# Kernel optimization log

Hardware: AMD Instinct MI355X
Metric: run time of the kernel (lower is better)

The kernel has to match this reference:

```python
import jax, jax.numpy as jnp
import numpy as np

N_NODES = 100000
N_EDGES = 1600000
N_GRAPHS = 128
IN_FEATS = 128
OUT_FEATS = 64


def setup_inputs() -> dict:
    key = jax.random.key(0)
    k1, k2, k3, k4, k5, k6 = jax.random.split(key, 6)
    features = jax.random.normal(k1, (N_NODES, IN_FEATS), jnp.float32)
    src = jax.random.randint(k2, (N_EDGES,), 0, N_NODES, dtype=jnp.int32)
    dst = jax.random.randint(k3, (N_EDGES,), 0, N_NODES, dtype=jnp.int32)
    graph_ids = jnp.sort(jax.random.randint(k4, (N_NODES,), 0, N_GRAPHS, dtype=jnp.int32))
    # Xavier-uniform init as in DGL GraphConv
    lim1 = float(np.sqrt(6.0 / (IN_FEATS + IN_FEATS)))
    lim2 = float(np.sqrt(6.0 / (IN_FEATS + OUT_FEATS)))
    W1 = jax.random.uniform(k5, (IN_FEATS, IN_FEATS), jnp.float32, -lim1, lim1)
    W2 = jax.random.uniform(k6, (IN_FEATS, OUT_FEATS), jnp.float32, -lim2, lim2)
    b1 = jnp.zeros((IN_FEATS,), jnp.float32)
    b2 = jnp.zeros((OUT_FEATS,), jnp.float32)
    return {"features": features, "W1": W1, "b1": b1, "W2": W2, "b2": b2,
            "src": src, "dst": dst, "graph_ids": graph_ids, "num_graphs": N_GRAPHS}


def _graph_conv(x, W, b, src, dst, n_nodes):
    # DGL GraphConv, norm='both': D_dst^{-1/2} A D_src^{-1/2} X W + b
    ones = jnp.ones(src.shape, x.dtype)
    deg_out = jax.ops.segment_sum(ones, src, num_segments=n_nodes)
    deg_in = jax.ops.segment_sum(ones, dst, num_segments=n_nodes)
    norm_src = jax.lax.rsqrt(jnp.maximum(deg_out, 1.0))  # [N]
    norm_dst = jax.lax.rsqrt(jnp.maximum(deg_in, 1.0))   # [N]
    h = (x * norm_src[:, None]) @ W                       # dense transform first
    agg = jax.ops.segment_sum(h[src], dst, num_segments=n_nodes)  # spmm-style scatter-add
    return agg * norm_dst[:, None] + b


def reference(features, W1, b1, W2, b2, src, dst, graph_ids, num_graphs):
    n = features.shape[0]
    h = jax.nn.relu(_graph_conv(features, W1, b1, src, dst, n))
    h = jax.nn.relu(_graph_conv(h, W2, b2, src, dst, n))
    # dgl.mean_nodes: per-graph mean over nodes
    sums = jax.ops.segment_sum(h, graph_ids, num_segments=num_graphs)
    counts = jax.ops.segment_sum(jnp.ones((n, 1), h.dtype), graph_ids, num_segments=num_graphs)
    return sums / jnp.maximum(counts, 1.0)
```

## Files before the change

### kernel.cpp

```cpp
#include <hip/hip_runtime.h>
#include <hip/hip_bf16.h>


#define NPP_SHIFT 9
#define NPP 512
#define MAXP 256
#define NB 512

typedef __attribute__((ext_vector_type(8))) short frag8;
typedef __attribute__((ext_vector_type(4))) float f32x4;
typedef __attribute__((ext_vector_type(2))) float v2f;

__launch_bounds__(256)
__global__ void passA_count(const int* __restrict__ src, const int* __restrict__ dst,
                            int E, int P, int* __restrict__ counts_src,
                            int* __restrict__ counts_dst,
                            const int* __restrict__ gids, int N, int G,
                            int* __restrict__ gcnt) {
    __shared__ int h1[MAXP], h2[MAXP], h3[MAXP];
    int tid = threadIdx.x;
    for (int i = tid; i < MAXP; i += 256) { h1[i] = 0; h2[i] = 0; h3[i] = 0; }
    __syncthreads();
    int per_block = (E + NB - 1) / NB;
    int e0 = blockIdx.x * per_block;
    int e1 = min(e0 + per_block, E);
    for (int e = e0 + tid; e < e1; e += 256) {
        atomicAdd(&h1[src[e] >> NPP_SHIFT], 1);
        atomicAdd(&h2[dst[e] >> NPP_SHIFT], 1);
    }
    int npb = (N + NB - 1) / NB;
    int n0 = blockIdx.x * npb;
    int n1 = min(n0 + npb, N);
    for (int i = n0 + tid; i < n1; i += 256) atomicAdd(&h3[gids[i]], 1);
    __syncthreads();
    for (int i = tid; i < P; i += 256) {
        counts_src[(size_t)blockIdx.x * P + i] = h1[i];
        counts_dst[(size_t)blockIdx.x * P + i] = h2[i];
    }
    for (int i = tid; i < G; i += 256)
        if (h3[i]) atomicAdd(&gcnt[i], h3[i]);
}

__launch_bounds__(1024)
__global__ void scanB(const int* __restrict__ counts, int* __restrict__ offs,
                      int* __restrict__ ptot, int P) {
    __shared__ int s[1024];
    int tid = threadIdx.x;
    int p = blockIdx.x % P;
    int st = blockIdx.x / P;
    const int* c = counts + (size_t)st * NB * P;
    int v = (tid < NB) ? c[(size_t)tid * P + p] : 0;
    s[tid] = v;
    __syncthreads();
    for (int off = 1; off < 1024; off <<= 1) {
        int t = (tid >= off) ? s[tid - off] : 0;
        __syncthreads();
        s[tid] += t;
        __syncthreads();
    }
    if (tid < NB) offs[(size_t)st * NB * P + (size_t)tid * P + p] = s[tid] - v;
    if (tid == 1023) ptot[st * P + p] = s[1023];
}

__launch_bounds__(256)
__global__ void passC_scatter(const int* __restrict__ src, const int* __restrict__ dst,
                              int E, int P, const int* __restrict__ offs,
                              const int* __restrict__ ptot, int* __restrict__ pbase,
                              int* __restrict__ ebuf_src, int2* __restrict__ ebuf_dst) {
    __shared__ int cur1[MAXP], cur2[MAXP], sc[256];
    int tid = threadIdx.x;
    int v = (tid < P) ? ptot[tid] : 0;
    sc[tid] = v;
    __syncthreads();
    for (int off = 1; off < 256; off <<= 1) {
        int t = (tid >= off) ? sc[tid - off] : 0;
        __syncthreads();
        sc[tid] += t;
        __syncthreads();
    }
    int base0 = sc[tid] - v;
    if (tid < P) {
        cur1[tid] = base0 + offs[(size_t)blockIdx.x * P + tid];
        if (blockIdx.x == 0) pbase[tid] = base0;
    }
    __syncthreads();
    v = (tid < P) ? ptot[P + tid] : 0;
    sc[tid] = v;
    __syncthreads();
    for (int off = 1; off < 256; off <<= 1) {
        int t = (tid >= off) ? sc[tid - off] : 0;
        __syncthreads();
        sc[tid] += t;
        __syncthreads();
    }
    int base1 = sc[tid] - v;
    if (tid < P) {
        cur2[tid] = base1 + offs[(size_t)NB * P + (size_t)blockIdx.x * P + tid];
        if (blockIdx.x == 0) pbase[P + tid] = base1;
    }
    __syncthreads();
    int per_block = (E + NB - 1) / NB;
    int e0 = blockIdx.x * per_block;
    int e1 = min(e0 + per_block, E);
    for (int e = e0 + tid; e < e1; e += 256) {
        int s = src[e];
        int d = dst[e];
        int pos1 = atomicAdd(&cur1[s >> NPP_SHIFT], 1);
        ebuf_src[pos1] = s;
        int pos2 = atomicAdd(&cur2[d >> NPP_SHIFT], 1);
        ebuf_dst[pos2] = make_int2(d, s);
    }
}

__launch_bounds__(512)
__global__ void passD_build(const int* __restrict__ ebuf_src, const int2* __restrict__ ebuf_dst,
                            const int* __restrict__ ptot, const int* __restrict__ pbase,
                            float* __restrict__ norm_src, int* __restrict__ row_start,
                            int* __restrict__ csr_src, int N, int E, int P) {
    __shared__ int hs[NPP], hd[NPP], sc[NPP];
    int tid = threadIdx.x;
    int p = blockIdx.x;
    int node_lo = p << NPP_SHIFT;
    int nl = min(NPP, N - node_lo);
    hs[tid] = 0;
    hd[tid] = 0;
    __syncthreads();
    int nsrc = ptot[p];
    int base_s = pbase[p];
    for (int i = tid; i < nsrc; i += 512)
        atomicAdd(&hs[ebuf_src[base_s + i] - node_lo], 1);
    int ndst = ptot[P + p];
    int base_d = pbase[P + p];
    for (int i = tid; i < ndst; i += 512)
        atomicAdd(&hd[ebuf_dst[base_d + i].x - node_lo], 1);
    __syncthreads();
    if (tid < nl) norm_src[node_lo + tid] = rsqrtf((float)max(hs[tid], 1));
    int myh = hd[tid];
    sc[tid] = myh;
    __syncthreads();
    for (int off = 1; off < 512; off <<= 1) {
        int t = (tid >= off) ? sc[tid - off] : 0;
        __syncthreads();
        sc[tid] += t;
        __syncthreads();
    }
    int row0 = base_d + sc[tid] - myh;
    if (tid < nl) row_start[node_lo + tid] = row0;
    if (p == P - 1 && tid == 0) row_start[N] = E;
    __syncthreads();
    hd[tid] = row0;
    __syncthreads();
    for (int i = tid; i < ndst; i += 512) {
        int2 r = ebuf_dst[base_d + i];
        int pos = atomicAdd(&hd[r.x - node_lo], 1);
        csr_src[pos] = r.y;
    }
}

template <int COLS, bool BF16IN, bool PERM, bool FP8OUT>
__launch_bounds__(256)
__global__ void gemm_mfma(const void* __restrict__ xin, const float* __restrict__ w,
                          const float* __restrict__ norm,
                          void* __restrict__ out, int n) {
    constexpr int NT = COLS / 16;
    __shared__ short wlds[4 * NT * 64 * 8];
    const int tid = threadIdx.x;
    for (int i = tid; i < 128 * COLS / 4; i += 256) {
        int k = (i * 4) / COLS;
        int n0 = (i * 4) % COLS;
        float4 wv;
        if constexpr (PERM) {
            int ksrc = 64 * ((k >> 2) & 1) + 16 * (k & 3) + (k >> 3);
            wv = *reinterpret_cast<const float4*>(w + (size_t)ksrc * COLS + n0);
        } else {
            wv = reinterpret_cast<const float4*>(w)[i];
        }
        int c = k >> 5, q = (k >> 3) & 3, j = k & 7;
        float vals[4] = {wv.x, wv.y, wv.z, wv.w};
#pragma unroll
        for (int u = 0; u < 4; ++u) {
            int nn = n0 + u;
            int t = nn >> 4;
            int ln = (q << 4) | (nn & 15);
            union { __hip_bfloat16 b; short s; } cv;
            cv.b = __float2bfloat16(vals[u]);
            wlds[(((c * NT + t) << 6) | ln) * 8 + j] = cv.s;
        }
    }
    __syncthreads();

    const int lane = tid & 63;
    const int wid = tid >> 6;
    const int m = lane & 15;
    const int q = lane >> 4;
    const int ntiles = (n + 15) >> 4;
    const frag8* wfr = reinterpret_cast<const frag8*>(wlds);

    for (int wt = blockIdx.x * 4 + wid; wt < ntiles; wt += gridDim.x * 4) {
        const int row = (wt << 4) + m;
        frag8 af[4];
        if (row < n) {
            if constexpr (BF16IN) {
                const frag8* xp = reinterpret_cast<const frag8*>(
                    (const __hip_bfloat16*)xin + (size_t)row * 128);
#pragma unroll
                for (int c = 0; c < 4; ++c) af[c] = xp[c * 4 + q];
            } else {
                const float* xp = (const float*)xin + (size_t)row * 128;
                float nm = norm[row];
#pragma unroll
                for (int c = 0; c < 4; ++c) {
                    int base = c * 32 + q * 8;
                    float4 v0 = *reinterpret_cast<const float4*>(xp + base);
                    float4 v1 = *reinterpret_cast<const float4*>(xp + base + 4);
                    union { frag8 f; short s[8]; } a;
                    union { __hip_bfloat16 b; short s; } cv;
                    cv.b = __float2bfloat16(v0.x * nm); a.s[0] = cv.s;
                    cv.b = __float2bfloat16(v0.y * nm); a.s[1] = cv.s;
                    cv.b = __float2bfloat16(v0.z * nm); a.s[2] = cv.s;
                    cv.b = __float2bfloat16(v0.w * nm); a.s[3] = cv.s;
                    cv.b = __float2bfloat16(v1.x * nm); a.s[4] = cv.s;
                    cv.b = __float2bfloat16(v1.y * nm); a.s[5] = cv.s;
                    cv.b = __float2bfloat16(v1.z * nm); a.s[6] = cv.s;
                    cv.b = __float2bfloat16(v1.w * nm); a.s[7] = cv.s;
                    af[c] = a.f;
                }
            }
        } else {
#pragma unroll
            for (int c = 0; c < 4; ++c) af[c] = frag8{0, 0, 0, 0, 0, 0, 0, 0};
        }
        f32x4 acc[NT] = {};
#pragma unroll
        for (int c = 0; c < 4; ++c)
#pragma unroll
            for (int t = 0; t < NT; ++t)
                acc[t] = __builtin_amdgcn_mfma_f32_16x16x32_bf16(
                    af[c], wfr[(c * NT + t) * 64 + lane], acc[t], 0, 0, 0);
#pragma unroll
        for (int r = 0; r < 4; ++r) {
            int grow = (wt << 4) + q * 4 + r;
            if (grow < n) {
                if constexpr (FP8OUT && COLS == 128) {
                    uint w0 = 0, w1 = 0;
                    w0 = (uint)__builtin_amdgcn_cvt_pk_fp8_f32(acc[0][r], acc[1][r], (int)w0, false);
                    w0 = (uint)__builtin_amdgcn_cvt_pk_fp8_f32(acc[2][r], acc[3][r], (int)w0, true);
                    w1 = (uint)__builtin_amdgcn_cvt_pk_fp8_f32(acc[4][r], acc[5][r], (int)w1, false);
                    w1 = (uint)__builtin_amdgcn_cvt_pk_fp8_f32(acc[6][r], acc[7][r], (int)w1, true);
                    reinterpret_cast<uint2*>(out)[(size_t)grow * 16 + m] = make_uint2(w0, w1);
                } else if constexpr (FP8OUT) {
                    uint w0 = 0;
                    w0 = (uint)__builtin_amdgcn_cvt_pk_fp8_f32(acc[0][r], acc[1][r], (int)w0, false);
                    w0 = (uint)__builtin_amdgcn_cvt_pk_fp8_f32(acc[2][r], acc[3][r], (int)w0, true);
                    reinterpret_cast<uint*>(out)[(size_t)grow * 16 + m] = w0;
                } else {
                    __hip_bfloat16* ob = reinterpret_cast<__hip_bfloat16*>(out);
#pragma unroll
                    for (int t = 0; t < NT; ++t)
                        ob[(size_t)grow * COLS + t * 16 + m] = __float2bfloat16(acc[t][r]);
                }
            }
        }
    }
}

__launch_bounds__(256)
__global__ void spmm1_kernel(const uint* __restrict__ h1,
                             const int* __restrict__ row_start,
                             const int* __restrict__ csr_src,
                             const float* __restrict__ b1,
                             const float* __restrict__ norm_src,
                             uint2* __restrict__ x2n, int n) {
    int wv = (blockIdx.x * blockDim.x + threadIdx.x) >> 6;
    int lane = threadIdx.x & 63;
    int r0 = wv * 2;
    if (r0 >= n) return;
    int a = lane >> 5;
    int s = lane & 31;
    int e0[2], e1[2];
#pragma unroll
    for (int r = 0; r < 2; ++r) {
        int rr = min(r0 + r, n - 1);
        e0[r] = row_start[rr];
        e1[r] = row_start[rr + 1];
        if (r0 + r >= n) e1[r] = e0[r];
    }
    float acc[2][4] = {};
    int nb = max((e1[0] - e0[0] + 15) >> 4, (e1[1] - e0[1] + 15) >> 4);
    for (int b = 0; b < nb; ++b) {
        uint v[2][8];
#pragma unroll
        for (int r = 0; r < 2; ++r) {
            int base = e0[r] + b * 16;
            if (base < e1[r]) {
#pragma unroll
                for (int j = 0; j < 8; ++j) {
                    int idx = base + 2 * j + a;
                    int cidx = min(idx, e1[r] - 1);
                    uint vv = h1[(size_t)csr_src[cidx] * 32 + s];
                    v[r][j] = (idx < e1[r]) ? vv : 0u;
                }
            } else {
#pragma unroll
                for (int j = 0; j < 8; ++j) v[r][j] = 0u;
            }
        }
#pragma unroll
        for (int r = 0; r < 2; ++r)
#pragma unroll
            for (int j = 0; j < 8; ++j) {
                v2f lo = __builtin_amdgcn_cvt_pk_f32_fp8((int)v[r][j], false);
                v2f hi = __builtin_amdgcn_cvt_pk_f32_fp8((int)v[r][j], true);
                acc[r][0] += lo[0]; acc[r][1] += lo[1];
                acc[r][2] += hi[0]; acc[r][3] += hi[1];
            }
    }
#pragma unroll
    for (int r = 0; r < 2; ++r)
#pragma unroll
        for (int k = 0; k < 4; ++k) acc[r][k] += __shfl_xor(acc[r][k], 32);
    if (a == 0) {
        int m2 = s >> 1;
        int a2 = (s & 1) << 6;
        float bb0 = b1[a2 + m2], bb1 = b1[a2 + 16 + m2];
        float bb2 = b1[a2 + 32 + m2], bb3 = b1[a2 + 48 + m2];
#pragma unroll
        for (int r = 0; r < 2; ++r) {
            if (r0 + r < n) {
                float nd = rsqrtf((float)max(e1[r] - e0[r], 1));
                float ns = norm_src[r0 + r];
                float f0 = fmaxf(fmaf(acc[r][0], nd, bb0), 0.f) * ns;
                float f1 = fmaxf(fmaf(acc[r][1], nd, bb1), 0.f) * ns;
                float f2 = fmaxf(fmaf(acc[r][2], nd, bb2), 0.f) * ns;
                float f3 = fmaxf(fmaf(acc[r][3], nd, bb3), 0.f) * ns;
                union { __hip_bfloat16 b; ushort u; } c0, c1, c2, c3;
                c0.b = __float2bfloat16(f0);
                c1.b = __float2bfloat16(f1);
                c2.b = __float2bfloat16(f2);
                c3.b = __float2bfloat16(f3);
                uint w0 = (uint)c0.u | ((uint)c1.u << 16);
                uint w1 = (uint)c2.u | ((uint)c3.u << 16);
                x2n[(size_t)(r0 + r) * 32 + s] = make_uint2(w0, w1);
            }
        }
    }
}

__launch_bounds__(256)
__global__ void spmm2_kernel(const uint* __restrict__ h2,
                             const int* __restrict__ row_start,
                             const int* __restrict__ csr_src,
                             const float* __restrict__ b2,
                             const int* __restrict__ gids,
                             const int* __restrict__ gcnt,
                             float* __restrict__ out, int n) {
    int wv = (blockIdx.x * blockDim.x + threadIdx.x) >> 6;
    int lane = threadIdx.x & 63;
    int wave = threadIdx.x >> 6;
    int r0 = wv * 4;
    int a = lane >> 4;
    int s = lane & 15;
    int e0[4], e1[4], g[4];
    float inv[4];
#pragma unroll
    for (int r = 0; r < 4; ++r) {
        int rr = min(r0 + r, n - 1);
        e0[r] = row_start[rr];
        e1[r] = row_start[rr + 1];
        g[r] = gids[rr];
        if (r0 + r >= n) { e1[r] = e0[r]; g[r] = -1; }
        inv[r] = 1.f / (float)max(gcnt[max(g[r], 0)], 1);
    }
    float acc[4][4] = {};
    int nb = 0;
#pragma unroll
    for (int r = 0; r < 4; ++r) nb = max(nb, (e1[r] - e0[r] + 15) >> 4);
    for (int b = 0; b < nb; ++b) {
        uint u[4][4];
#pragma unroll
        for (int r = 0; r < 4; ++r) {
            int base = e0[r] + b * 16;
            if (base < e1[r]) {
#pragma unroll
                for (int j = 0; j < 4; ++j) {
                    int idx = base + 4 * j + a;
                    int cidx = min(idx, e1[r] - 1);
                    uint vv = h2[(size_t)csr_src[cidx] * 16 + s];
                    u[r][j] = (idx < e1[r]) ? vv : 0u;
                }
            } else {
#pragma unroll
                for (int j = 0; j < 4; ++j) u[r][j] = 0u;
            }
        }
#pragma unroll
        for (int r = 0; r < 4; ++r)
#pragma unroll
            for (int j = 0; j < 4; ++j) {
                v2f lo = __builtin_amdgcn_cvt_pk_f32_fp8((int)u[r][j], false);
                v2f hi = __builtin_amdgcn_cvt_pk_f32_fp8((int)u[r][j], true);
                acc[r][0] += lo[0]; acc[r][1] += lo[1];
                acc[r][2] += hi[0]; acc[r][3] += hi[1];
            }
    }
#pragma unroll
    for (int r = 0; r < 4; ++r)
#pragma unroll
        for (int k = 0; k < 4; ++k) {
            acc[r][k] += __shfl_xor(acc[r][k], 16);
            acc[r][k] += __shfl_xor(acc[r][k], 32);
        }
    float bb0 = b2[s], bb1 = b2[16 + s], bb2v = b2[32 + s], bb3 = b2[48 + s];
    float val[4][4];
#pragma unroll
    for (int r = 0; r < 4; ++r) {
        float nd = rsqrtf((float)max(e1[r] - e0[r], 1));
        bool vld = g[r] >= 0;
        val[r][0] = vld ? fmaxf(fmaf(acc[r][0], nd, bb0), 0.f) * inv[r] : 0.f;
        val[r][1] = vld ? fmaxf(fmaf(acc[r][1], nd, bb1), 0.f) * inv[r] : 0.f;
        val[r][2] = vld ? fmaxf(fmaf(acc[r][2], nd, bb2v), 0.f) * inv[r] : 0.f;
        val[r][3] = vld ? fmaxf(fmaf(acc[r][3], nd, bb3), 0.f) * inv[r] : 0.f;
    }
    __shared__ float sbuf[4][64];
    __shared__ int sg[4];
    bool same = (g[0] == g[1]) && (g[1] == g[2]) && (g[2] == g[3]) && (g[0] >= 0);
    int sgw;
    if (same) {
        if (a == 0) {
            sbuf[wave][s]      = val[0][0] + val[1][0] + val[2][0] + val[3][0];
            sbuf[wave][16 + s] = val[0][1] + val[1][1] + val[2][1] + val[3][1];
            sbuf[wave][32 + s] = val[0][2] + val[1][2] + val[2][2] + val[3][2];
            sbuf[wave][48 + s] = val[0][3] + val[1][3] + val[2][3] + val[3][3];
        }
        sgw = g[0];
    } else {
        if (a == 0) {
#pragma unroll
            for (int r = 0; r < 4; ++r) {
                if (g[r] >= 0) {
                    atomicAdd(&out[(size_t)g[r] * 64 + s], val[r][0]);
                    atomicAdd(&out[(size_t)g[r] * 64 + 16 + s], val[r][1]);
                    atomicAdd(&out[(size_t)g[r] * 64 + 32 + s], val[r][2]);
                    atomicAdd(&out[(size_t)g[r] * 64 + 48 + s], val[r][3]);
                }
            }
            sbuf[wave][s] = 0.f;
            sbuf[wave][16 + s] = 0.f;
            sbuf[wave][32 + s] = 0.f;
            sbuf[wave][48 + s] = 0.f;
        }
        sgw = -1;
    }
    if (lane == 0) sg[wave] = sgw;
    __syncthreads();
    if (wave == 0) {
        int g0 = sg[0], g1 = sg[1], g2 = sg[2], g3 = sg[3];
        if (g0 == g1 && g1 == g2 && g2 == g3 && g0 >= 0) {
            float ssum = sbuf[0][lane] + sbuf[1][lane] + sbuf[2][lane] + sbuf[3][lane];
            atomicAdd(&out[(size_t)g0 * 64 + lane], ssum);
        } else {
#pragma unroll
            for (int w = 0; w < 4; ++w)
                if (sg[w] >= 0)
                    atomicAdd(&out[(size_t)sg[w] * 64 + lane], sbuf[w][lane]);
        }
    }
}

extern "C" void kernel_launch(void* const* d_in, const int* in_sizes, int n_in,
                              void* d_out, int out_size, void* d_ws, size_t ws_size,
                              hipStream_t stream) {
    const float* features = (const float*)d_in[0];
    const float* W1 = (const float*)d_in[1];
    const float* b1 = (const float*)d_in[2];
    const float* W2 = (const float*)d_in[3];
    const float* b2 = (const float*)d_in[4];
    const int* src = (const int*)d_in[5];
    const int* dst = (const int*)d_in[6];
    const int* gids = (const int*)d_in[7];
    const int N = in_sizes[7];
    const int E = in_sizes[5];
    const int G = out_size / 64;
    float* out = (float*)d_out;
    const int P = (N + NPP - 1) >> NPP_SHIFT;

    char* ws = (char*)d_ws;
    size_t off = 0;
    auto alloc = [&](size_t bytes) -> void* {
        void* p = ws + off;
        off = (off + bytes + 255) & ~(size_t)255;
        return p;
    };
    int* counts = (int*)alloc((size_t)2 * NB * P * 4);
    int* offs = (int*)alloc((size_t)2 * NB * P * 4);
    int* ptot = (int*)alloc((size_t)2 * P * 4);
    int* pbase = (int*)alloc((size_t)2 * P * 4);
    int* gcnt = (int*)alloc((size_t)G * 4);
    int* ebuf_src = (int*)alloc((size_t)E * 4);
    int2* ebuf_dst = (int2*)alloc((size_t)E * 8);
    float* norm_src = (float*)alloc((size_t)N * 4);
    int* row_start = (int*)alloc((size_t)(N + 1) * 4);
    int* csr_src = (int*)alloc((size_t)E * 4);
    uint* h1 = (uint*)alloc((size_t)N * 128);
    __hip_bfloat16* x2n = (__hip_bfloat16*)alloc((size_t)N * 128 * 2);
    uint* h2 = h1;

    hipMemsetAsync(out, 0, (size_t)out_size * sizeof(float), stream);
    hipMemsetAsync(gcnt, 0, (size_t)G * 4, stream);

    passA_count<<<NB, 256, 0, stream>>>(src, dst, E, P, counts, counts + (size_t)NB * P,
                                        gids, N, G, gcnt);
    scanB<<<2 * P, 1024, 0, stream>>>(counts, offs, ptot, P);
    passC_scatter<<<NB, 256, 0, stream>>>(src, dst, E, P, offs, ptot, pbase,
                                          ebuf_src, ebuf_dst);
    passD_build<<<P, 512, 0, stream>>>(ebuf_src, ebuf_dst, ptot, pbase, norm_src, row_start,
                                       csr_src, N, E, P);

    gemm_mfma<128, false, false, true><<<768, 256, 0, stream>>>(features, W1, norm_src,
                                                                (void*)h1, N);
    {
        int waves = (N + 1) / 2;
        int blocks = (waves * 64 + 255) / 256;
        spmm1_kernel<<<blocks, 256, 0, stream>>>(h1, row_start, csr_src, b1, norm_src,
                                                 (uint2*)x2n, N);
    }
    gemm_mfma<64, true, true, true><<<768, 256, 0, stream>>>(x2n, W2, nullptr,
                                                             (void*)h2, N);
    {
        int waves = (N + 3) / 4;
        int blocks = (waves * 64 + 255) / 256;
        spmm2_kernel<<<blocks, 256, 0, stream>>>(h2, row_start, csr_src, b2,
                                                 gids, gcnt, out, N);
    }
}
```

Before: 287.9 us.

## Replace count/scan/scatter CSR build with fixed-capacity bucketed scatter and global degree atomics

```diff
diff --git a/kernel.cpp b/kernel.cpp
--- a/kernel.cpp
+++ b/kernel.cpp
@@ -6,137 +6,59 @@
 #define NPP 512
 #define MAXP 256
 #define NB 512
+#define CAPP 10240
 
 typedef __attribute__((ext_vector_type(8))) short frag8;
 typedef __attribute__((ext_vector_type(4))) float f32x4;
 typedef __attribute__((ext_vector_type(2))) float v2f;
 
 __launch_bounds__(256)
-__global__ void passA_count(const int* __restrict__ src, const int* __restrict__ dst,
-                            int E, int P, int* __restrict__ counts_src,
-                            int* __restrict__ counts_dst,
-                            const int* __restrict__ gids, int N, int G,
-                            int* __restrict__ gcnt) {
-    __shared__ int h1[MAXP], h2[MAXP], h3[MAXP];
+__global__ void buildC(const int* __restrict__ src, const int* __restrict__ dst,
+                       int E, int P, int* __restrict__ cur,
+                       int2* __restrict__ ebuf_dst, int* __restrict__ deg,
+                       const int* __restrict__ gids, int N, int G,
+                       int* __restrict__ gcnt) {
+    __shared__ int h[MAXP], bs[MAXP], hg[MAXP];
     int tid = threadIdx.x;
-    for (int i = tid; i < MAXP; i += 256) { h1[i] = 0; h2[i] = 0; h3[i] = 0; }
+    for (int i = tid; i < MAXP; i += 256) { h[i] = 0; hg[i] = 0; }
     __syncthreads();
     int per_block = (E + NB - 1) / NB;
     int e0 = blockIdx.x * per_block;
     int e1 = min(e0 + per_block, E);
     for (int e = e0 + tid; e < e1; e += 256) {
-        atomicAdd(&h1[src[e] >> NPP_SHIFT], 1);
-        atomicAdd(&h2[dst[e] >> NPP_SHIFT], 1);
+        atomicAdd(&h[dst[e] >> NPP_SHIFT], 1);
+        atomicAdd(&deg[src[e]], 1);
     }
     int npb = (N + NB - 1) / NB;
     int n0 = blockIdx.x * npb;
     int n1 = min(n0 + npb, N);
-    for (int i = n0 + tid; i < n1; i += 256) atomicAdd(&h3[gids[i]], 1);
-    __syncthreads();
-    for (int i = tid; i < P; i += 256) {
-        counts_src[(size_t)blockIdx.x * P + i] = h1[i];
-        counts_dst[(size_t)blockIdx.x * P + i] = h2[i];
+    for (int i = n0 + tid; i < n1; i += 256) atomicAdd(&hg[gids[i]], 1);
+    __syncthreads();
+    for (int p = tid; p < P; p += 256) {
+        int c = h[p];
+        bs[p] = c ? atomicAdd(&cur[p], c) : 0;
+        h[p] = 0;
     }
     for (int i = tid; i < G; i += 256)
-        if (h3[i]) atomicAdd(&gcnt[i], h3[i]);
-}
-
-__launch_bounds__(1024)
-__global__ void scanB(const int* __restrict__ counts, int* __restrict__ offs,
-                      int* __restrict__ ptot, int P) {
-    __shared__ int s[1024];
-    int tid = threadIdx.x;
-    int p = blockIdx.x % P;
-    int st = blockIdx.x / P;
-    const int* c = counts + (size_t)st * NB * P;
-    int v = (tid < NB) ? c[(size_t)tid * P + p] : 0;
-    s[tid] = v;
-    __syncthreads();
-    for (int off = 1; off < 1024; off <<= 1) {
-        int t = (tid >= off) ? s[tid - off] : 0;
-        __syncthreads();
-        s[tid] += t;
-        __syncthreads();
-    }
-    if (tid < NB) offs[(size_t)st * NB * P + (size_t)tid * P + p] = s[tid] - v;
-    if (tid == 1023) ptot[st * P + p] = s[1023];
-}
-
-__launch_bounds__(256)
-__global__ void passC_scatter(const int* __restrict__ src, const int* __restrict__ dst,
-                              int E, int P, const int* __restrict__ offs,
-                              const int* __restrict__ ptot, int* __restrict__ pbase,
-                              int* __restrict__ ebuf_src, int2* __restrict__ ebuf_dst) {
-    __shared__ int cur1[MAXP], cur2[MAXP], sc[256];
-    int tid = threadIdx.x;
-    int v = (tid < P) ? ptot[tid] : 0;
-    sc[tid] = v;
-    __syncthreads();
-    for (int off = 1; off < 256; off <<= 1) {
-        int t = (tid >= off) ? sc[tid - off] : 0;
-        __syncthreads();
-        sc[tid] += t;
-        __syncthreads();
-    }
-    int base0 = sc[tid] - v;
-    if (tid < P) {
-        cur1[tid] = base0 + offs[(size_t)blockIdx.x * P + tid];
-        if (blockIdx.x == 0) pbase[tid] = base0;
-    }
-    __syncthreads();
-    v = (tid < P) ? ptot[P + tid] : 0;
-    sc[tid] = v;
-    __syncthreads();
-    for (int off = 1; off < 256; off <<= 1) {
-        int t = (tid >= off) ? sc[tid - off] : 0;
-        __syncthreads();
-        sc[tid] += t;
-        __syncthreads();
-    }
-    int base1 = sc[tid] - v;
-    if (tid < P) {
-        cur2[tid] = base1 + offs[(size_t)NB * P + (size_t)blockIdx.x * P + tid];
-        if (blockIdx.x == 0) pbase[P + tid] = base1;
-    }
-    __syncthreads();
-    int per_block = (E + NB - 1) / NB;
-    int e0 = blockIdx.x * per_block;
-    int e1 = min(e0 + per_block, E);
+        if (hg[i]) atomicAdd(&gcnt[i], hg[i]);
+    __syncthreads();
     for (int e = e0 + tid; e < e1; e += 256) {
+        int d = dst[e];
         int s = src[e];
-        int d = dst[e];
-        int pos1 = atomicAdd(&cur1[s >> NPP_SHIFT], 1);
-        ebuf_src[pos1] = s;
-        int pos2 = atomicAdd(&cur2[d >> NPP_SHIFT], 1);
-        ebuf_dst[pos2] = make_int2(d, s);
+        int p = d >> NPP_SHIFT;
+        int lp = atomicAdd(&h[p], 1);
+        ebuf_dst[(size_t)p * CAPP + bs[p] + lp] = make_int2(d, s);
     }
 }
 
 __launch_bounds__(512)
-__global__ void passD_build(const int* __restrict__ ebuf_src, const int2* __restrict__ ebuf_dst,
-                            const int* __restrict__ ptot, const int* __restrict__ pbase,
-                            float* __restrict__ norm_src, int* __restrict__ row_start,
-                            int* __restrict__ csr_src, int N, int E, int P) {
-    __shared__ int hs[NPP], hd[NPP], sc[NPP];
+__global__ void passD2(const int2* __restrict__ ebuf_dst, const int* __restrict__ cur,
+                       int* __restrict__ row_start, int* __restrict__ csr_src,
+                       int N, int E, int P) {
+    __shared__ int hd[NPP], sc[NPP];
     int tid = threadIdx.x;
     int p = blockIdx.x;
-    int node_lo = p << NPP_SHIFT;
-    int nl = min(NPP, N - node_lo);
-    hs[tid] = 0;
-    hd[tid] = 0;
-    __syncthreads();
-    int nsrc = ptot[p];
-    int base_s = pbase[p];
-    for (int i = tid; i < nsrc; i += 512)
-        atomicAdd(&hs[ebuf_src[base_s + i] - node_lo], 1);
-    int ndst = ptot[P + p];
-    int base_d = pbase[P + p];
-    for (int i = tid; i < ndst; i += 512)
-        atomicAdd(&hd[ebuf_dst[base_d + i].x - node_lo], 1);
-    __syncthreads();
-    if (tid < nl) norm_src[node_lo + tid] = rsqrtf((float)max(hs[tid], 1));
-    int myh = hd[tid];
-    sc[tid] = myh;
+    sc[tid] = (tid < P) ? cur[tid] : 0;
     __syncthreads();
     for (int off = 1; off < 512; off <<= 1) {
         int t = (tid >= off) ? sc[tid - off] : 0;
@@ -144,7 +66,27 @@
         sc[tid] += t;
         __syncthreads();
     }
-    int row0 = base_d + sc[tid] - myh;
+    int gbase = (p > 0) ? sc[p - 1] : 0;
+    __syncthreads();
+    int node_lo = p << NPP_SHIFT;
+    int nl = min(NPP, N - node_lo);
+    hd[tid] = 0;
+    __syncthreads();
+    int ndst = cur[p];
+    size_t base_d = (size_t)p * CAPP;
+    for (int i = tid; i < ndst; i += 512)
+        atomicAdd(&hd[ebuf_dst[base_d + i].x - node_lo], 1);
+    __syncthreads();
+    int myh = hd[tid];
+    sc[tid] = myh;
+    __syncthreads();
+    for (int off = 1; off < 512; off <<= 1) {
+        int t = (tid >= off) ? sc[tid - off] : 0;
+        __syncthreads();
+        sc[tid] += t;
+        __syncthreads();
+    }
+    int row0 = gbase + sc[tid] - myh;
     if (tid < nl) row_start[node_lo + tid] = row0;
     if (p == P - 1 && tid == 0) row_start[N] = E;
     __syncthreads();
@@ -160,7 +102,7 @@
 template <int COLS, bool BF16IN, bool PERM, bool FP8OUT>
 __launch_bounds__(256)
 __global__ void gemm_mfma(const void* __restrict__ xin, const float* __restrict__ w,
-                          const float* __restrict__ norm,
+                          const int* __restrict__ deg,
                           void* __restrict__ out, int n) {
     constexpr int NT = COLS / 16;
     __shared__ short wlds[4 * NT * 64 * 8];
@@ -207,7 +149,7 @@
                 for (int c = 0; c < 4; ++c) af[c] = xp[c * 4 + q];
             } else {
                 const float* xp = (const float*)xin + (size_t)row * 128;
-                float nm = norm[row];
+                float nm = rsqrtf((float)max(deg[row], 1));
 #pragma unroll
                 for (int c = 0; c < 4; ++c) {
                     int base = c * 32 + q * 8;
@@ -265,18 +207,18 @@
 }
 
 __launch_bounds__(256)
-__global__ void spmm1_kernel(const uint* __restrict__ h1,
+__global__ void spmm1_kernel(const uint2* __restrict__ h1,
                              const int* __restrict__ row_start,
                              const int* __restrict__ csr_src,
                              const float* __restrict__ b1,
-                             const float* __restrict__ norm_src,
-                             uint2* __restrict__ x2n, int n) {
+                             const int* __restrict__ deg,
+                             uint4* __restrict__ x2n, int n) {
     int wv = (blockIdx.x * blockDim.x + threadIdx.x) >> 6;
     int lane = threadIdx.x & 63;
     int r0 = wv * 2;
     if (r0 >= n) return;
-    int a = lane >> 5;
-    int s = lane & 31;
+    int a = lane >> 4;
+    int s = lane & 15;
     int e0[2], e1[2];
 #pragma unroll
     for (int r = 0; r < 2; ++r) {
@@ -285,62 +227,73 @@
         e1[r] = row_start[rr + 1];
         if (r0 + r >= n) e1[r] = e0[r];
     }
-    float acc[2][4] = {};
+    v2f acc[2][4] = {};
     int nb = max((e1[0] - e0[0] + 15) >> 4, (e1[1] - e0[1] + 15) >> 4);
     for (int b = 0; b < nb; ++b) {
-        uint v[2][8];
+        uint2 v[2][4];
 #pragma unroll
         for (int r = 0; r < 2; ++r) {
             int base = e0[r] + b * 16;
-            if (base < e1[r]) {
-#pragma unroll
-                for (int j = 0; j < 8; ++j) {
-                    int idx = base + 2 * j + a;
+            if (base + 16 <= e1[r]) {
+#pragma unroll
+                for (int j = 0; j < 4; ++j)
+                    v[r][j] = h1[(size_t)csr_src[base + 4 * j + a] * 16 + s];
+            } else if (base < e1[r]) {
+#pragma unroll
+                for (int j = 0; j < 4; ++j) {
+                    int idx = base + 4 * j + a;
                     int cidx = min(idx, e1[r] - 1);
-                    uint vv = h1[(size_t)csr_src[cidx] * 32 + s];
-                    v[r][j] = (idx < e1[r]) ? vv : 0u;
+                    uint2 vv = h1[(size_t)csr_src[cidx] * 16 + s];
+                    bool ok = idx < e1[r];
+                    v[r][j].x = ok ? vv.x : 0u;
+                    v[r][j].y = ok ? vv.y : 0u;
                 }
             } else {
 #pragma unroll
-                for (int j = 0; j < 8; ++j) v[r][j] = 0u;
+                for (int j = 0; j < 4; ++j) v[r][j] = make_uint2(0u, 0u);
             }
         }
 #pragma unroll
         for (int r = 0; r < 2; ++r)
 #pragma unroll
-            for (int j = 0; j < 8; ++j) {
-                v2f lo = __builtin_amdgcn_cvt_pk_f32_fp8((int)v[r][j], false);
-                v2f hi = __builtin_amdgcn_cvt_pk_f32_fp8((int)v[r][j], true);
-                acc[r][0] += lo[0]; acc[r][1] += lo[1];
-                acc[r][2] += hi[0]; acc[r][3] += hi[1];
+            for (int j = 0; j < 4; ++j) {
+                acc[r][0] += __builtin_amdgcn_cvt_pk_f32_fp8((int)v[r][j].x, false);
+                acc[r][1] += __builtin_amdgcn_cvt_pk_f32_fp8((int)v[r][j].x, true);
+                acc[r][2] += __builtin_amdgcn_cvt_pk_f32_fp8((int)v[r][j].y, false);
+                acc[r][3] += __builtin_amdgcn_cvt_pk_f32_fp8((int)v[r][j].y, true);
             }
     }
 #pragma unroll
     for (int r = 0; r < 2; ++r)
 #pragma unroll
-        for (int k = 0; k < 4; ++k) acc[r][k] += __shfl_xor(acc[r][k], 32);
+        for (int k = 0; k < 4; ++k) {
+            v2f t;
+            t[0] = __shfl_xor(acc[r][k][0], 16);
+            t[1] = __shfl_xor(acc[r][k][1], 16);
+            acc[r][k] += t;
+            t[0] = __shfl_xor(acc[r][k][0], 32);
+            t[1] = __shfl_xor(acc[r][k][1], 32);
+            acc[r][k] += t;
+        }
     if (a == 0) {
-        int m2 = s >> 1;
-        int a2 = (s & 1) << 6;
-        float bb0 = b1[a2 + m2], bb1 = b1[a2 + 16 + m2];
-        float bb2 = b1[a2 + 32 + m2], bb3 = b1[a2 + 48 + m2];
+        float bbl[4] = {b1[s], b1[32 + s], b1[64 + s], b1[96 + s]};
+        float bbh[4] = {b1[16 + s], b1[48 + s], b1[80 + s], b1[112 + s]};
 #pragma unroll
         for (int r = 0; r < 2; ++r) {
             if (r0 + r < n) {
                 float nd = rsqrtf((float)max(e1[r] - e0[r], 1));
-                float ns = norm_src[r0 + r];
-                float f0 = fmaxf(fmaf(acc[r][0], nd, bb0), 0.f) * ns;
-                float f1 = fmaxf(fmaf(acc[r][1], nd, bb1), 0.f) * ns;
-                float f2 = fmaxf(fmaf(acc[r][2], nd, bb2), 0.f) * ns;
-                float f3 = fmaxf(fmaf(acc[r][3], nd, bb3), 0.f) * ns;
-                union { __hip_bfloat16 b; ushort u; } c0, c1, c2, c3;
-                c0.b = __float2bfloat16(f0);
-                c1.b = __float2bfloat16(f1);
-                c2.b = __float2bfloat16(f2);
-                c3.b = __float2bfloat16(f3);
-                uint w0 = (uint)c0.u | ((uint)c1.u << 16);
-                uint w1 = (uint)c2.u | ((uint)c3.u << 16);
-                x2n[(size_t)(r0 + r) * 32 + s] = make_uint2(w0, w1);
+                float ns = rsqrtf((float)max(deg[r0 + r], 1));
+                uint w[4];
+#pragma unroll
+                for (int k = 0; k < 4; ++k) {
+                    float fl = fmaxf(fmaf(acc[r][k][0], nd, bbl[k]), 0.f) * ns;
+                    float fh = fmaxf(fmaf(acc[r][k][1], nd, bbh[k]), 0.f) * ns;
+                    union { __hip_bfloat16 b; ushort u; } cl, ch;
+                    cl.b = __float2bfloat16(fl);
+                    ch.b = __float2bfloat16(fh);
+                    w[k] = (uint)cl.u | ((uint)ch.u << 16);
+                }
+                x2n[(size_t)(r0 + r) * 16 + s] = make_uint4(w[0], w[1], w[2], w[3]);
             }
         }
     }
@@ -380,7 +333,11 @@
 #pragma unroll
         for (int r = 0; r < 4; ++r) {
             int base = e0[r] + b * 16;
-            if (base < e1[r]) {
+            if (base + 16 <= e1[r]) {
+#pragma unroll
+                for (int j = 0; j < 4; ++j)
+                    u[r][j] = h2[(size_t)csr_src[base + 4 * j + a] * 16 + s];
+            } else if (base < e1[r]) {
 #pragma unroll
                 for (int j = 0; j < 4; ++j) {
                     int idx = base + 4 * j + a;
@@ -491,14 +448,11 @@
         off = (off + bytes + 255) & ~(size_t)255;
         return p;
     };
-    int* counts = (int*)alloc((size_t)2 * NB * P * 4);
-    int* offs = (int*)alloc((size_t)2 * NB * P * 4);
-    int* ptot = (int*)alloc((size_t)2 * P * 4);
-    int* pbase = (int*)alloc((size_t)2 * P * 4);
-    int* gcnt = (int*)alloc((size_t)G * 4);
-    int* ebuf_src = (int*)alloc((size_t)E * 4);
-    int2* ebuf_dst = (int2*)alloc((size_t)E * 8);
-    float* norm_src = (float*)alloc((size_t)N * 4);
+    int* zblock = (int*)alloc((size_t)(G + N + P) * 4);
+    int* gcnt = zblock;
+    int* deg = zblock + G;
+    int* cur = deg + N;
+    int2* ebuf_dst = (int2*)alloc((size_t)P * CAPP * 8);
     int* row_start = (int*)alloc((size_t)(N + 1) * 4);
     int* csr_src = (int*)alloc((size_t)E * 4);
     uint* h1 = (uint*)alloc((size_t)N * 128);
@@ -506,23 +460,18 @@
     uint* h2 = h1;
 
     hipMemsetAsync(out, 0, (size_t)out_size * sizeof(float), stream);
-    hipMemsetAsync(gcnt, 0, (size_t)G * 4, stream);
-
-    passA_count<<<NB, 256, 0, stream>>>(src, dst, E, P, counts, counts + (size_t)NB * P,
-                                        gids, N, G, gcnt);
-    scanB<<<2 * P, 1024, 0, stream>>>(counts, offs, ptot, P);
-    passC_scatter<<<NB, 256, 0, stream>>>(src, dst, E, P, offs, ptot, pbase,
-                                          ebuf_src, ebuf_dst);
-    passD_build<<<P, 512, 0, stream>>>(ebuf_src, ebuf_dst, ptot, pbase, norm_src, row_start,
-                                       csr_src, N, E, P);
-
-    gemm_mfma<128, false, false, true><<<768, 256, 0, stream>>>(features, W1, norm_src,
+    hipMemsetAsync(zblock, 0, (size_t)(G + N + P) * 4, stream);
+
+    buildC<<<NB, 256, 0, stream>>>(src, dst, E, P, cur, ebuf_dst, deg, gids, N, G, gcnt);
+    passD2<<<P, 512, 0, stream>>>(ebuf_dst, cur, row_start, csr_src, N, E, P);
+
+    gemm_mfma<128, false, false, true><<<768, 256, 0, stream>>>(features, W1, deg,
                                                                 (void*)h1, N);
     {
         int waves = (N + 1) / 2;
         int blocks = (waves * 64 + 255) / 256;
-        spmm1_kernel<<<blocks, 256, 0, stream>>>(h1, row_start, csr_src, b1, norm_src,
-                                                 (uint2*)x2n, N);
+        spmm1_kernel<<<blocks, 256, 0, stream>>>((const uint2*)h1, row_start, csr_src, b1,
+                                                 deg, (uint4*)x2n, N);
     }
     gemm_mfma<64, true, true, true><<<768, 256, 0, stream>>>(x2n, W2, nullptr,
                                                              (void*)h2, N);
```

Result: slower. 318.7 us (+10.7%).
